# Kernel tuning notes

Measured on AMD Instinct MI355X. Metric: run time of the kernel, lower is better.

Reference implementation:

```python
import jax, jax.numpy as jnp
import numpy as np

B, S, D, H = 8, 512, 1024, 16
HD = D // H                      # head_dim = 64
MAX_SEQ_LEN = 512
SCRATCH_SLOTS = 64


def _rope_cache():
    inv_freq = 1.0 / (10000.0 ** (jnp.arange(0, HD, 2, dtype=jnp.float32) / HD))
    t = jnp.arange(MAX_SEQ_LEN + SCRATCH_SLOTS, dtype=jnp.float32)
    freqs = jnp.outer(t, inv_freq)               # [T, HD//2]
    freqs = jnp.concatenate([freqs, freqs], -1)  # [T, HD]
    return jnp.sin(freqs), jnp.cos(freqs)


def rotate_half(x):
    x1, x2 = x[..., : x.shape[-1] // 2], x[..., x.shape[-1] // 2 :]
    return jnp.concatenate([-x2, x1], axis=-1)


def setup_inputs() -> dict:
    key = jax.random.key(0)
    ks = jax.random.split(key, 5)
    def w(k):
        return jax.random.normal(k, (D, D), dtype=jnp.float32) * 0.02
    return {
        "x": jax.random.normal(ks[0], (B, S, D), dtype=jnp.float32),
        "Wq": w(ks[1]), "bq": jnp.zeros((D,), jnp.float32),
        "Wk": w(ks[2]), "bk": jnp.zeros((D,), jnp.float32),
        "Wv": w(ks[3]), "bv": jnp.zeros((D,), jnp.float32),
        "Wo": w(ks[4]), "bo": jnp.zeros((D,), jnp.float32),
    }


def reference(x, Wq, bq, Wk, bk, Wv, bv, Wo, bo):
    b, s, d = x.shape
    sin_c, cos_c = _rope_cache()
    scale = jnp.array(HD ** (-0.5), dtype=jnp.float32)

    xh = x.astype(jnp.float16)
    def lin(inp, W, bias):  # nnx.Linear with dtype=fp16: cast params + input to fp16
        return inp @ W.astype(jnp.float16) + bias.astype(jnp.float16)

    q = lin(xh, Wq, bq).reshape(b, s, H, HD)
    k = lin(xh, Wk, bk).reshape(b, s, H, HD)
    v = lin(xh, Wv, bv).reshape(b, s, H, HD)

    sin = sin_c[:s, None, :].astype(jnp.float32)  # [s,1,HD]
    cos = cos_c[:s, None, :].astype(jnp.float32)
    qf = q.astype(jnp.float32)
    kf = k.astype(jnp.float32)
    q = qf * cos + rotate_half(qf) * sin
    k = kf * cos + rotate_half(kf) * sin
    v = v.astype(jnp.float32)
    q = q * scale  # module's explicit scale

    # [b,H,s,HD]
    q, k, v = (t.transpose(0, 2, 1, 3) for t in (q, k, v))

    # jax.nn.dot_product_attention additionally scales by 1/sqrt(HD)
    logits = jnp.einsum("bhqd,bhkd->bhqk", q, k) * scale
    probs = jax.nn.softmax(logits, axis=-1)
    out = jnp.einsum("bhqk,bhkd->bhqd", probs, v)
    out = out.transpose(0, 2, 1, 3).reshape(b, s, d)
    return lin(out.astype(jnp.float16), Wo, bo)
```

## Files before the change

kernel.cpp:

```cpp
#include <hip/hip_runtime.h>

typedef _Float16 half8 __attribute__((ext_vector_type(8)));
typedef _Float16 half4v __attribute__((ext_vector_type(4)));
typedef float f32x4 __attribute__((ext_vector_type(4)));

#define OFF_CS    0u
#define OFF_XH    (1u<<20)
#define OFF_WQKVT (OFF_XH + 8u*1024u*1024u)
#define OFF_WOT   (OFF_WQKVT + 8u*1024u*1024u)
#define OFF_QKV   (OFF_WOT + 2u*1024u*1024u)
#define OFF_VT    OFF_XH
#define OFF_ATTN  OFF_WQKVT

__device__ __forceinline__ void gload16(const _Float16* g, _Float16* l) {
  __builtin_amdgcn_global_load_lds((const __attribute__((address_space(1))) void*)g,
                                   (__attribute__((address_space(3))) void*)l, 16, 0, 0);
}

__global__ void prep_k(const float* __restrict__ x,
                       const float* __restrict__ W0, const float* __restrict__ W1,
                       const float* __restrict__ W2, const float* __restrict__ W3,
                       _Float16* __restrict__ xh, _Float16* __restrict__ wqkvt,
                       _Float16* __restrict__ wot, float2* __restrict__ cs) {
  int bid = blockIdx.x, tid = threadIdx.x;
  if (bid < 4096) {
    int i = bid * 256 + tid;
    float4 v = ((const float4*)x)[i];
    half4v h;
    h[0] = (_Float16)v.x; h[1] = (_Float16)v.y; h[2] = (_Float16)v.z; h[3] = (_Float16)v.w;
    *(half4v*)(xh + (size_t)i * 4) = h;
  } else if (bid < 8192) {
    __shared__ float tile[32][33];
    int tb = bid - 4096;
    int z = tb >> 10, t = tb & 1023, by = t >> 5, bx = t & 31;
    const float* W = z == 0 ? W0 : z == 1 ? W1 : z == 2 ? W2 : W3;
    _Float16* Wt = z < 3 ? wqkvt + (size_t)z * 1048576 : wot;
    int r = tid >> 3, c0 = (tid & 7) * 4;
    float4 v = *(const float4*)(W + (size_t)(by * 32 + r) * 1024 + bx * 32 + c0);
    tile[r][c0] = v.x; tile[r][c0 + 1] = v.y; tile[r][c0 + 2] = v.z; tile[r][c0 + 3] = v.w;
    __syncthreads();
    half4v h;
#pragma unroll
    for (int j = 0; j < 4; j++) h[j] = (_Float16)tile[c0 + j][r];
    *(half4v*)(Wt + (size_t)(bx * 32 + r) * 1024 + by * 32 + c0) = h;
  } else {
    int idx = (bid - 8192) * 256 + tid;
    int pos = idx >> 5, j = idx & 31;
    float inv = powf(10000.0f, -(float)j * (1.0f / 32.0f));
    float f = (float)pos * inv;
    cs[idx] = make_float2(cosf(f), sinf(f));
  }
}

template <int MODE>
__global__ __launch_bounds__(256, MODE == 0 ? 3 : 2) void gemm_k(
    const _Float16* __restrict__ A, const _Float16* __restrict__ Bt,
    const float* __restrict__ b0, const float* __restrict__ b1, const float* __restrict__ b2,
    void* __restrict__ Cv, const float2* __restrict__ cs) {
  constexpr int BM  = (MODE == 0) ? 128 : 64;
  constexpr int N   = (MODE == 0) ? 3072 : 1024;
  constexpr int NBX = N / 128;
  constexpr int MF  = BM / 32;
  constexpr int ACH = BM / 64;
  __shared__ _Float16 Ar[3][BM * 32];
  __shared__ _Float16 Br[3][128 * 32];

  int nwg = gridDim.x, cpx = nwg >> 3;
  int bid = blockIdx.x;
  int wgid = (bid & 7) * cpx + (bid >> 3);
  int by = wgid / NBX, bx = wgid % NBX;

  int tid = threadIdx.x, lane = tid & 63, w = tid >> 6;
  int wr = w >> 1, wc = w & 1;
  int arow = lane & 15, ag = lane >> 4;
  int s8 = (((arow & 1) << 2) | ag) ^ ((arow >> 1) & 7);

  int qq = (lane & 7) ^ (lane >> 3);
  int rloc = ((lane >> 3) << 1) + (qq >> 2);
  int gcol = (qq & 3) * 8;

  const _Float16* Ag = A + (size_t)(by * BM) * 1024;
  const _Float16* Bg = Bt + (size_t)(bx * 128) * 1024;

  f32x4 acc[MF][4] = {};

  auto stage = [&](int t) {
    int slot = t % 3;
    int k0 = t * 32;
#pragma unroll
    for (int i = 0; i < ACH; i++) {
      int c = w * ACH + i;
      gload16(Ag + (size_t)(c * 16 + rloc) * 1024 + k0 + gcol, &Ar[slot][c * 512]);
    }
#pragma unroll
    for (int i = 0; i < 2; i++) {
      int c = w * 2 + i;
      gload16(Bg + (size_t)(c * 16 + rloc) * 1024 + k0 + gcol, &Br[slot][c * 512]);
    }
  };

  stage(0); stage(1);
  if (MODE == 0) asm volatile("s_waitcnt vmcnt(4)" ::: "memory");
  else           asm volatile("s_waitcnt vmcnt(3)" ::: "memory");
  __builtin_amdgcn_s_barrier();
  __builtin_amdgcn_sched_barrier(0);

  for (int t = 0; t < 32; ++t) {
    if (t < 30) stage(t + 2);
    __builtin_amdgcn_sched_barrier(0);
    const _Float16* Ac = &Ar[t % 3][0];
    const _Float16* Bc = &Br[t % 3][0];
    half8 a[MF], b[4];
#pragma unroll
    for (int m = 0; m < MF; m++) {
      int R = wr * (BM / 2) + m * 16 + arow;
      a[m] = *(const half8*)&Ac[(R >> 1) * 64 + s8 * 8];
    }
#pragma unroll
    for (int n = 0; n < 4; n++) {
      int R = wc * 64 + n * 16 + arow;
      b[n] = *(const half8*)&Bc[(R >> 1) * 64 + s8 * 8];
    }
    __builtin_amdgcn_s_setprio(1);
#pragma unroll
    for (int m = 0; m < MF; m++)
#pragma unroll
      for (int n = 0; n < 4; n++)
        acc[m][n] = __builtin_amdgcn_mfma_f32_16x16x32_f16(a[m], b[n], acc[m][n], 0, 0, 0);
    __builtin_amdgcn_s_setprio(0);
    __builtin_amdgcn_sched_barrier(0);
    if (t < 30) {
      if (MODE == 0) asm volatile("s_waitcnt vmcnt(4)" ::: "memory");
      else           asm volatile("s_waitcnt vmcnt(3)" ::: "memory");
    } else if (t == 30) {
      asm volatile("s_waitcnt vmcnt(0)" ::: "memory");
    }
    if (t < 31) {
      __builtin_amdgcn_s_barrier();
      __builtin_amdgcn_sched_barrier(0);
    }
  }

  int gc0 = bx * 128 + wc * 64;
  if (MODE == 0) {
    const float* bp = gc0 < 1024 ? b0 : (gc0 < 2048 ? b1 : b2);
    float bb_[4];
#pragma unroll
    for (int n = 0; n < 4; n++) bb_[n] = bp[(gc0 & 1023) + n * 16 + arow];
    _Float16* C = (_Float16*)Cv;
    if (gc0 < 2048) {
      bool isQ = gc0 < 1024;
#pragma unroll
      for (int m = 0; m < MF; m++) {
        int gr = by * BM + wr * (BM / 2) + m * 16 + ag * 4;
#pragma unroll
        for (int r = 0; r < 4; r++) {
          int row = gr + r, pos = row & 511;
#pragma unroll
          for (int n = 0; n < 2; n++) {
            int j = n * 16 + arow;
            float av = (float)(_Float16)(acc[m][n][r] + bb_[n]);
            float bv = (float)(_Float16)(acc[m][n + 2][r] + bb_[n + 2]);
            float2 tt = cs[pos * 32 + j];
            float o0 = av * tt.x - bv * tt.y;
            float o1 = bv * tt.x + av * tt.y;
            if (isQ) { o0 *= 0.015625f; o1 *= 0.015625f; }
            C[(size_t)row * 3072 + gc0 + j]      = (_Float16)o0;
            C[(size_t)row * 3072 + gc0 + j + 32] = (_Float16)o1;
          }
        }
      }
    } else {
#pragma unroll
      for (int m = 0; m < MF; m++) {
        int gr = by * BM + wr * (BM / 2) + m * 16 + ag * 4;
#pragma unroll
        for (int n = 0; n < 4; n++)
#pragma unroll
          for (int r = 0; r < 4; r++)
            C[(size_t)(gr + r) * 3072 + gc0 + n * 16 + arow] = (_Float16)(acc[m][n][r] + bb_[n]);
      }
    }
  } else {
    float* C = (float*)Cv;
#pragma unroll
    for (int m = 0; m < MF; m++) {
      int gr = by * BM + wr * (BM / 2) + m * 16 + ag * 4;
#pragma unroll
      for (int n = 0; n < 4; n++) {
        int gc = gc0 + n * 16 + arow;
        float bb = b0[gc];
#pragma unroll
        for (int r = 0; r < 4; r++)
          C[(size_t)(gr + r) * 1024 + gc] = (float)(_Float16)(acc[m][n][r] + bb);
      }
    }
  }
}

__global__ void vt_k(const _Float16* __restrict__ qkv, _Float16* __restrict__ VT) {
  __shared__ _Float16 T[64][72];
  int id = blockIdx.x;
  int bh = id & 127, sb = id >> 7;
  int b = bh >> 4, h = bh & 15;
  int tid = threadIdx.x;
  const _Float16* src = qkv + (size_t)(b * 512 + sb * 64) * 3072 + 2048 + h * 64;
#pragma unroll
  for (int i = 0; i < 2; i++) {
    int c = i * 256 + tid, r = c >> 3, cc = c & 7;
    *(half8*)&T[r][cc * 8] = *(const half8*)(src + (size_t)r * 3072 + cc * 8);
  }
  __syncthreads();
  _Float16* dst = VT + (size_t)bh * 64 * 512 + (size_t)sb * 64;
#pragma unroll
  for (int i = 0; i < 2; i++) {
    int c = i * 256 + tid, hd = c >> 3, sc = c & 7;
    half8 v;
#pragma unroll
    for (int j = 0; j < 8; j++) v[j] = T[sc * 8 + j][hd];
    *(half8*)(dst + (size_t)hd * 512 + sc * 8) = v;
  }
}

__global__ __launch_bounds__(256, 4) void attn_k(const _Float16* __restrict__ qkv,
                                                 const _Float16* __restrict__ VT,
                                                 _Float16* __restrict__ out) {
  int id = blockIdx.x;
  int bh = id & 127, qt = id >> 7;
  int b = bh >> 4, h = bh & 15;
  int tid = threadIdx.x, lane = tid & 63, w = tid >> 6;
  int arow = lane & 15, ag = lane >> 4;

  __shared__ _Float16 Kb2[2][64 * 64];
  __shared__ _Float16 Vs[64 * 64];
  __shared__ _Float16 Pl[4][16][72];

  int qrow0 = b * 512 + qt * 64 + w * 16;
  const _Float16* Qp = qkv + (size_t)qrow0 * 3072 + h * 64;
  half8 qa[2];
#pragma unroll
  for (int ks = 0; ks < 2; ks++)
    qa[ks] = *(const half8*)(Qp + (size_t)arow * 3072 + ks * 32 + ag * 8);

  const _Float16* Kg = qkv + (size_t)(b * 512) * 3072 + 1024 + h * 64;
  const _Float16* Vg = VT + (size_t)bh * 64 * 512;

  int srow = lane >> 3;
  int sslot = (lane & 7) ^ srow;
  const _Float16* Ksrc0 = Kg + (size_t)(w * 16 + srow) * 3072 + sslot * 8;
  const _Float16* Vsrc0 = Vg + (size_t)(w * 16 + srow) * 512 + sslot * 8;

  int rs = arow & 7;

  float psl[4] = {0.f, 0.f, 0.f, 0.f};
  f32x4 oacc[4] = {};

#pragma unroll
  for (int i = 0; i < 2; i++)
    gload16(Ksrc0 + (size_t)(i * 8) * 3072, &Kb2[0][(w * 16 + i * 8) * 64]);
  asm volatile("s_waitcnt vmcnt(0)" ::: "memory");
  __builtin_amdgcn_s_barrier();
  __builtin_amdgcn_sched_barrier(0);

  for (int st = 0; st < 8; ++st) {
#pragma unroll
    for (int i = 0; i < 2; i++)
      gload16(Vsrc0 + (size_t)(i * 8) * 512 + st * 64, &Vs[(w * 16 + i * 8) * 64]);
    if (st < 7) {
#pragma unroll
      for (int i = 0; i < 2; i++)
        gload16(Ksrc0 + (size_t)((st + 1) * 64 + i * 8) * 3072,
                &Kb2[(st + 1) & 1][(w * 16 + i * 8) * 64]);
    }
    __builtin_amdgcn_sched_barrier(0);
    const _Float16* Kc = &Kb2[st & 1][0];
    f32x4 lg[4];
#pragma unroll
    for (int c = 0; c < 4; c++) {
      f32x4 a0 = {};
      __builtin_amdgcn_s_setprio(1);
#pragma unroll
      for (int ks = 0; ks < 2; ks++) {
        int slot = (ks * 4 + ag) ^ rs;
        half8 kb = *(const half8*)&Kc[(c * 16 + arow) * 64 + slot * 8];
        a0 = __builtin_amdgcn_mfma_f32_16x16x32_f16(qa[ks], kb, a0, 0, 0, 0);
      }
      __builtin_amdgcn_s_setprio(0);
      lg[c] = a0;
    }
    _Float16 ph[4][4];
#pragma unroll
    for (int r = 0; r < 4; r++) {
#pragma unroll
      for (int c = 0; c < 4; c++) {
        float p = __builtin_amdgcn_exp2f(lg[c][r] * 1.44269504f);
        psl[r] += p;
        ph[c][r] = (_Float16)p;
      }
    }
#pragma unroll
    for (int c = 0; c < 4; c++)
#pragma unroll
      for (int r = 0; r < 4; r++) Pl[w][ag * 4 + r][c * 16 + arow] = ph[c][r];
    __builtin_amdgcn_sched_barrier(0);
    if (st < 7) asm volatile("s_waitcnt vmcnt(2)" ::: "memory");
    else        asm volatile("s_waitcnt vmcnt(0)" ::: "memory");
    __builtin_amdgcn_s_barrier();
    __builtin_amdgcn_sched_barrier(0);
#pragma unroll
    for (int ks = 0; ks < 2; ks++) {
      half8 pa = *(const half8*)&Pl[w][arow][ks * 32 + ag * 8];
      __builtin_amdgcn_s_setprio(1);
#pragma unroll
      for (int c = 0; c < 4; c++) {
        int slot = (ks * 4 + ag) ^ rs;
        half8 vb = *(const half8*)&Vs[(c * 16 + arow) * 64 + slot * 8];
        oacc[c] = __builtin_amdgcn_mfma_f32_16x16x32_f16(pa, vb, oacc[c], 0, 0, 0);
      }
      __builtin_amdgcn_s_setprio(0);
    }
    __builtin_amdgcn_sched_barrier(0);
    if (st < 7) {
      asm volatile("s_waitcnt vmcnt(0)" ::: "memory");
      __builtin_amdgcn_s_barrier();
      __builtin_amdgcn_sched_barrier(0);
    }
  }
#pragma unroll
  for (int r = 0; r < 4; r++)
#pragma unroll
    for (int d = 1; d < 16; d <<= 1) psl[r] += __shfl_xor(psl[r], d, 16);
#pragma unroll
  for (int c = 0; c < 4; c++)
#pragma unroll
    for (int r = 0; r < 4; r++) {
      float v = oacc[c][r] / psl[r];
      out[(size_t)(qrow0 + ag * 4 + r) * 1024 + h * 64 + c * 16 + arow] = (_Float16)v;
    }
}

extern "C" void kernel_launch(void* const* d_in, const int* in_sizes, int n_in,
                              void* d_out, int out_size, void* d_ws, size_t ws_size,
                              hipStream_t stream) {
  const float* x  = (const float*)d_in[0];
  const float* Wq = (const float*)d_in[1];
  const float* bq = (const float*)d_in[2];
  const float* Wk = (const float*)d_in[3];
  const float* bk = (const float*)d_in[4];
  const float* Wv = (const float*)d_in[5];
  const float* bv = (const float*)d_in[6];
  const float* Wo = (const float*)d_in[7];
  const float* bo = (const float*)d_in[8];

  char* ws = (char*)d_ws;
  float2* cs      = (float2*)(ws + OFF_CS);
  _Float16* xh    = (_Float16*)(ws + OFF_XH);
  _Float16* wqkvt = (_Float16*)(ws + OFF_WQKVT);
  _Float16* wot   = (_Float16*)(ws + OFF_WOT);
  _Float16* qkv   = (_Float16*)(ws + OFF_QKV);
  _Float16* VT    = (_Float16*)(ws + OFF_VT);
  _Float16* attn  = (_Float16*)(ws + OFF_ATTN);

  prep_k<<<8256, 256, 0, stream>>>(x, Wq, Wk, Wv, Wo, xh, wqkvt, wot, cs);
  gemm_k<0><<<768, 256, 0, stream>>>(xh, wqkvt, bq, bk, bv, qkv, cs);
  vt_k<<<1024, 256, 0, stream>>>(qkv, VT);
  attn_k<<<1024, 256, 0, stream>>>(qkv, VT, attn);
  gemm_k<1><<<512, 256, 0, stream>>>(attn, wot, bo, bo, bo, d_out, cs);
}
```

Before: 106.4 us.

## Fuse V transpose into QKV GEMM epilogue and drop the separate transpose kernel

The QKV GEMM epilogue now writes V straight into a transposed, tiled layout inside the qkv buffer, so the standalone vt_k transpose kernel and its extra read/write pass are gone. The attention kernel loads V tiles from this layout and drops the K double buffer, explicit waitcnt and setprio scheduling in favour of one buffer with __syncthreads. This saves a launch and a round trip through memory for V, but K loads are no longer prefetched ahead of use, which may expose load latency.

```diff
diff --git a/kernel.cpp b/kernel.cpp
--- a/kernel.cpp
+++ b/kernel.cpp
@@ -9,8 +9,8 @@
 #define OFF_WQKVT (OFF_XH + 8u*1024u*1024u)
 #define OFF_WOT   (OFF_WQKVT + 8u*1024u*1024u)
 #define OFF_QKV   (OFF_WOT + 2u*1024u*1024u)
-#define OFF_VT    OFF_XH
 #define OFF_ATTN  OFF_WQKVT
+
 
 __device__ __forceinline__ void gload16(const _Float16* g, _Float16* l) {
   __builtin_amdgcn_global_load_lds((const __attribute__((address_space(1))) void*)g,
@@ -174,11 +174,19 @@
 #pragma unroll
       for (int m = 0; m < MF; m++) {
         int gr = by * BM + wr * (BM / 2) + m * 16 + ag * 4;
-#pragma unroll
-        for (int n = 0; n < 4; n++)
-#pragma unroll
-          for (int r = 0; r < 4; r++)
-            C[(size_t)(gr + r) * 3072 + gc0 + n * 16 + arow] = (_Float16)(acc[m][n][r] + bb_[n]);
+        int bb2 = gr >> 9;
+        int st6 = (gr & 511) >> 6;
+        int s63 = gr & 63;
+#pragma unroll
+        for (int n = 0; n < 4; n++) {
+          int colh = gc0 - 2048 + n * 16 + arow;
+          int h = colh >> 6, hd = colh & 63;
+          half4v v4;
+#pragma unroll
+          for (int r = 0; r < 4; r++) v4[r] = (_Float16)(acc[m][n][r] + bb_[n]);
+          size_t addr = ((size_t)(bb2 * 512 + hd * 8 + st6)) * 3072 + 2048 + h * 64 + s63;
+          *(half4v*)(C + addr) = v4;
+        }
       }
     }
   } else {
@@ -198,32 +206,7 @@
   }
 }
 
-__global__ void vt_k(const _Float16* __restrict__ qkv, _Float16* __restrict__ VT) {
-  __shared__ _Float16 T[64][72];
-  int id = blockIdx.x;
-  int bh = id & 127, sb = id >> 7;
-  int b = bh >> 4, h = bh & 15;
-  int tid = threadIdx.x;
-  const _Float16* src = qkv + (size_t)(b * 512 + sb * 64) * 3072 + 2048 + h * 64;
-#pragma unroll
-  for (int i = 0; i < 2; i++) {
-    int c = i * 256 + tid, r = c >> 3, cc = c & 7;
-    *(half8*)&T[r][cc * 8] = *(const half8*)(src + (size_t)r * 3072 + cc * 8);
-  }
-  __syncthreads();
-  _Float16* dst = VT + (size_t)bh * 64 * 512 + (size_t)sb * 64;
-#pragma unroll
-  for (int i = 0; i < 2; i++) {
-    int c = i * 256 + tid, hd = c >> 3, sc = c & 7;
-    half8 v;
-#pragma unroll
-    for (int j = 0; j < 8; j++) v[j] = T[sc * 8 + j][hd];
-    *(half8*)(dst + (size_t)hd * 512 + sc * 8) = v;
-  }
-}
-
 __global__ __launch_bounds__(256, 4) void attn_k(const _Float16* __restrict__ qkv,
-                                                 const _Float16* __restrict__ VT,
                                                  _Float16* __restrict__ out) {
   int id = blockIdx.x;
   int bh = id & 127, qt = id >> 7;
@@ -231,7 +214,7 @@
   int tid = threadIdx.x, lane = tid & 63, w = tid >> 6;
   int arow = lane & 15, ag = lane >> 4;
 
-  __shared__ _Float16 Kb2[2][64 * 64];
+  __shared__ _Float16 Ks[64 * 64];
   __shared__ _Float16 Vs[64 * 64];
   __shared__ _Float16 Pl[4][16][72];
 
@@ -242,50 +225,37 @@
   for (int ks = 0; ks < 2; ks++)
     qa[ks] = *(const half8*)(Qp + (size_t)arow * 3072 + ks * 32 + ag * 8);
 
-  const _Float16* Kg = qkv + (size_t)(b * 512) * 3072 + 1024 + h * 64;
-  const _Float16* Vg = VT + (size_t)bh * 64 * 512;
+  const _Float16* Kb = qkv + (size_t)(b * 512) * 3072 + 1024 + h * 64;
 
   int srow = lane >> 3;
   int sslot = (lane & 7) ^ srow;
-  const _Float16* Ksrc0 = Kg + (size_t)(w * 16 + srow) * 3072 + sslot * 8;
-  const _Float16* Vsrc0 = Vg + (size_t)(w * 16 + srow) * 512 + sslot * 8;
+  const _Float16* Ksrc0 = Kb + (size_t)(w * 16 + srow) * 3072 + sslot * 8;
+  const _Float16* Vsrc0 = qkv + ((size_t)(b * 512) + (w * 16 + srow) * 8) * 3072
+                          + 2048 + h * 64 + sslot * 8;
 
   int rs = arow & 7;
 
   float psl[4] = {0.f, 0.f, 0.f, 0.f};
   f32x4 oacc[4] = {};
 
-#pragma unroll
-  for (int i = 0; i < 2; i++)
-    gload16(Ksrc0 + (size_t)(i * 8) * 3072, &Kb2[0][(w * 16 + i * 8) * 64]);
-  asm volatile("s_waitcnt vmcnt(0)" ::: "memory");
-  __builtin_amdgcn_s_barrier();
-  __builtin_amdgcn_sched_barrier(0);
-
   for (int st = 0; st < 8; ++st) {
 #pragma unroll
-    for (int i = 0; i < 2; i++)
-      gload16(Vsrc0 + (size_t)(i * 8) * 512 + st * 64, &Vs[(w * 16 + i * 8) * 64]);
-    if (st < 7) {
-#pragma unroll
-      for (int i = 0; i < 2; i++)
-        gload16(Ksrc0 + (size_t)((st + 1) * 64 + i * 8) * 3072,
-                &Kb2[(st + 1) & 1][(w * 16 + i * 8) * 64]);
-    }
-    __builtin_amdgcn_sched_barrier(0);
-    const _Float16* Kc = &Kb2[st & 1][0];
+    for (int i = 0; i < 2; i++) {
+      gload16(Ksrc0 + (size_t)(st * 64 + i * 8) * 3072, &Ks[(w * 16 + i * 8) * 64]);
+      gload16(Vsrc0 + (size_t)(i * 64 + st) * 3072,     &Vs[(w * 16 + i * 8) * 64]);
+    }
+    __syncthreads();
+
     f32x4 lg[4];
 #pragma unroll
     for (int c = 0; c < 4; c++) {
       f32x4 a0 = {};
-      __builtin_amdgcn_s_setprio(1);
 #pragma unroll
       for (int ks = 0; ks < 2; ks++) {
         int slot = (ks * 4 + ag) ^ rs;
-        half8 kb = *(const half8*)&Kc[(c * 16 + arow) * 64 + slot * 8];
+        half8 kb = *(const half8*)&Ks[(c * 16 + arow) * 64 + slot * 8];
         a0 = __builtin_amdgcn_mfma_f32_16x16x32_f16(qa[ks], kb, a0, 0, 0, 0);
       }
-      __builtin_amdgcn_s_setprio(0);
       lg[c] = a0;
     }
     _Float16 ph[4][4];
@@ -302,29 +272,17 @@
     for (int c = 0; c < 4; c++)
 #pragma unroll
       for (int r = 0; r < 4; r++) Pl[w][ag * 4 + r][c * 16 + arow] = ph[c][r];
-    __builtin_amdgcn_sched_barrier(0);
-    if (st < 7) asm volatile("s_waitcnt vmcnt(2)" ::: "memory");
-    else        asm volatile("s_waitcnt vmcnt(0)" ::: "memory");
-    __builtin_amdgcn_s_barrier();
-    __builtin_amdgcn_sched_barrier(0);
 #pragma unroll
     for (int ks = 0; ks < 2; ks++) {
       half8 pa = *(const half8*)&Pl[w][arow][ks * 32 + ag * 8];
-      __builtin_amdgcn_s_setprio(1);
 #pragma unroll
       for (int c = 0; c < 4; c++) {
         int slot = (ks * 4 + ag) ^ rs;
         half8 vb = *(const half8*)&Vs[(c * 16 + arow) * 64 + slot * 8];
         oacc[c] = __builtin_amdgcn_mfma_f32_16x16x32_f16(pa, vb, oacc[c], 0, 0, 0);
       }
-      __builtin_amdgcn_s_setprio(0);
-    }
-    __builtin_amdgcn_sched_barrier(0);
-    if (st < 7) {
-      asm volatile("s_waitcnt vmcnt(0)" ::: "memory");
-      __builtin_amdgcn_s_barrier();
-      __builtin_amdgcn_sched_barrier(0);
-    }
+    }
+    __syncthreads();
   }
 #pragma unroll
   for (int r = 0; r < 4; r++)
@@ -358,12 +316,10 @@
   _Float16* wqkvt = (_Float16*)(ws + OFF_WQKVT);
   _Float16* wot   = (_Float16*)(ws + OFF_WOT);
   _Float16* qkv   = (_Float16*)(ws + OFF_QKV);
-  _Float16* VT    = (_Float16*)(ws + OFF_VT);
   _Float16* attn  = (_Float16*)(ws + OFF_ATTN);
 
   prep_k<<<8256, 256, 0, stream>>>(x, Wq, Wk, Wv, Wo, xh, wqkvt, wot, cs);
   gemm_k<0><<<768, 256, 0, stream>>>(xh, wqkvt, bq, bk, bv, qkv, cs);
-  vt_k<<<1024, 256, 0, stream>>>(qkv, VT);
-  attn_k<<<1024, 256, 0, stream>>>(qkv, VT, attn);
+  attn_k<<<1024, 256, 0, stream>>>(qkv, attn);
   gemm_k<1><<<512, 256, 0, stream>>>(attn, wot, bo, bo, bo, d_out, cs);
 }
```

Result: faster. 90.79 us (median of 2 runs) (-14.7%).
